# Kernel tuning notes

Measured on AMD Instinct MI355X. Metric: run time of the kernel, lower is better.

The kernel has to match this reference:

```python
import jax, jax.numpy as jnp
import numpy as np

B = 1024
D_FEAT = 64
WINDOW_SIZE = 8192
IR_SIZE = 1024
MAX_STEPS = 2799.0


def setup_inputs() -> dict:
    key = jax.random.key(0)
    ks = jax.random.split(key, 8)
    d_in = D_FEAT + 1  # vel_inputs concat K
    return {
        "vel_inputs": jax.random.normal(ks[0], (B, D_FEAT), dtype=jnp.float32),
        "K": jax.random.uniform(ks[1], (B, 1), dtype=jnp.float32) * MAX_STEPS,
        "eps": jax.random.normal(ks[2], (B, WINDOW_SIZE), dtype=jnp.float32),
        "W_coeff": jax.random.normal(ks[3], (d_in, WINDOW_SIZE), dtype=jnp.float32) * 0.02,
        "b_coeff": jnp.zeros((WINDOW_SIZE,), jnp.float32),
        "W_amps": jax.random.normal(ks[4], (d_in, 1), dtype=jnp.float32) * 0.02,
        "b_amps": jnp.zeros((1,), jnp.float32),
        "W_mean": jax.random.normal(ks[5], (d_in, 1), dtype=jnp.float32) * 0.02,
        "b_mean": jnp.zeros((1,), jnp.float32),
    }


def reference(vel_inputs, K, eps, W_coeff, b_coeff, W_amps, b_amps, W_mean, b_mean):
    # --- small MLP heads ---
    x = jnp.concatenate([vel_inputs, K / MAX_STEPS], axis=-1)  # [B, D+1]
    noise_bands = x @ W_coeff + b_coeff                        # [B, W] (magnitudes)
    amps = jax.nn.sigmoid(x @ W_amps + b_amps)                 # [B, 1]
    mean = jnp.tanh(x @ W_mean + b_mean)                       # [B, 1]

    # --- frequency_impulse_response: irfft + hann windowing (padding>0 branch) ---
    ir = jnp.fft.irfft(noise_bands, axis=-1)   # [B, 2*(W-1)] real
    ir = jnp.fft.fftshift(ir, axes=-1)
    ir_len = 2 * (WINDOW_SIZE - 1)             # 16382
    half = (IR_SIZE + 1) // 2                  # 512
    pad = ir_len - IR_SIZE                     # > 0 path
    n = jnp.arange(IR_SIZE, dtype=jnp.float32)
    hann = 0.5 - 0.5 * jnp.cos(2.0 * jnp.pi * n / IR_SIZE)  # tf periodic hann
    window = jnp.concatenate([hann[half:], jnp.zeros((pad,), jnp.float32), hann[:half]])
    ir = window * ir
    fhs = ir_len - (half - 1) + 1              # first_half_start
    she = half + 1                             # second_half_end
    impulse = jnp.concatenate([ir[:, fhs:], ir[:, :she]], axis=-1)  # [B, IR_SIZE-1]
    ir_final = impulse.shape[-1]               # 1023

    # --- noise generation (eps ~ N(0,1) injected for determinism) ---
    noise = mean + eps                         # [B, W]
    noise = noise / jnp.max(noise)             # global max, as in tf code

    # --- fft_convolve: original broadcasts to [B,B,...] then takes [0];
    # equivalent: noise row 0 convolved with every batch's impulse. ---
    conv_len = ir_final + WINDOW_SIZE - 1
    fft_size = int(2 ** np.ceil(np.log2(conv_len)))  # 16384
    a_fft = jnp.fft.rfft(noise[0], n=fft_size)          # [F]
    ir_fft = jnp.fft.rfft(impulse, n=fft_size, axis=-1)  # [B, F]
    conv = jnp.fft.irfft(a_fft[None, :] * ir_fft, axis=-1)  # [B, fft_size]

    # crop_and_compensate_delay ('same')
    start = (ir_final - 1) // 2 - 1            # 510
    cropped = conv[:, start:start + WINDOW_SIZE]  # [B, W]

    # overlap_and_add over a single frame with step W//2 is the identity
    out_noise = amps * cropped                 # [B, W]
    return out_noise, mean
```

## Files before the change

### kernel.cpp

```cpp
#include <hip/hip_runtime.h>
#include <math.h>

#define NB 1024
#define DF 64
#define WIN 8192
#define LIR 16382
#define TBASE 7681
#define NJ 1024
#define INV_MAXSTEPS (1.0f/2799.0f)
#define TWO_PI 6.28318530717958647692f

#define REVLEN 9248
#define SREV 8212

#define BW_ELEMS 1160
#define BW_CHUNKS 145

using short8 = __attribute__((ext_vector_type(8))) short;
using f32x4  = __attribute__((ext_vector_type(4))) float;

static __device__ __forceinline__ short f2bf(float x) {
    unsigned u = __float_as_uint(x);
    unsigned r = (u + 0x7fffu + ((u >> 16) & 1u)) >> 16;
    return (short)r;
}

#define PREP_CT_BLK 4096
#define PREP_W_BLK  320
#define PREP_H_BLK  4
__global__ __launch_bounds__(256) void k_prep(const float* __restrict__ Wc,
                                              const float* __restrict__ bc,
                                              const float* __restrict__ vel,
                                              const float* __restrict__ Kv,
                                              const float* __restrict__ Wa,
                                              const float* __restrict__ ba,
                                              const float* __restrict__ Wm,
                                              const float* __restrict__ bm,
                                              short* __restrict__ Ct,
                                              short* __restrict__ Waug,
                                              float* __restrict__ amps,
                                              float* __restrict__ mean,
                                              float* __restrict__ out_mean,
                                              unsigned* __restrict__ gmb) {
    int bx = blockIdx.x, tid = threadIdx.x;
    if (bx < PREP_CT_BLK) {
        int flat = bx * 2048 + tid * 8;
        int j = flat >> 13, k0 = flat & 8191;
        int t = TBASE + j;
        int p = (k0 * t) % LIR;
        float hw = 0.5f - 0.5f * __builtin_amdgcn_cosf((float)(j + 2) * (1.0f / 1024.0f));
        if (j == NJ - 1) hw = 0.0f;
        short8 v;
        #pragma unroll
        for (int e = 0; e < 8; ++e) {
            int k = k0 + e;
            float w = (k == 0 || k == LIR / 2) ? (1.0f / (float)LIR) : (2.0f / (float)LIR);
            float c = __builtin_amdgcn_cosf((float)p * (1.0f / (float)LIR)) * w * hw;
            v[e] = f2bf(c);
            p += t; if (p >= LIR) p -= LIR;
        }
        *(short8*)(Ct + flat) = v;
    } else if (bx < PREP_CT_BLK + PREP_W_BLK) {
        int flat = (bx - PREP_CT_BLK) * 2048 + tid * 8;
        int d = flat >> 13, k0 = flat & 8191;
        short8 v;
        #pragma unroll
        for (int e = 0; e < 8; ++e) {
            float x = 0.0f;
            if (d < 65)       x = Wc[(size_t)d * WIN + k0 + e];
            else if (d == 65) x = bc[k0 + e];
            v[e] = f2bf(x);
        }
        *(short8*)(Waug + flat) = v;
    } else if (bx < PREP_CT_BLK + PREP_W_BLK + PREP_H_BLK) {
        int b = (bx - PREP_CT_BLK - PREP_W_BLK) * 256 + tid;
        float sa = ba[0], sm = bm[0];
        #pragma unroll 8
        for (int d = 0; d < DF; ++d) {
            float v = vel[b * DF + d];
            sa = fmaf(v, Wa[d], sa);
            sm = fmaf(v, Wm[d], sm);
        }
        float xk = Kv[b] * INV_MAXSTEPS;
        sa = fmaf(xk, Wa[DF], sa);
        sm = fmaf(xk, Wm[DF], sm);
        amps[b] = 1.0f / (1.0f + expf(-sa));
        float m = tanhf(sm);
        mean[b] = m;
        out_mean[b] = m;
    } else {
        if (tid == 0) gmb[0] = 0u;
    }
}

__global__ void k_maxpart(const float* __restrict__ eps, const float* __restrict__ mean,
                          unsigned* __restrict__ gmb) {
    __shared__ float red[256];
    int tid = threadIdx.x;
    float m = -INFINITY;
    const int total4 = NB * WIN / 4;
    const int stride = 1024 * 256;
    const float4* e4 = (const float4*)eps;
    for (int idx = blockIdx.x * 256 + tid; idx < total4; idx += stride) {
        int b = idx >> 11;
        float4 v = e4[idx];
        float mm = fmaxf(fmaxf(v.x, v.y), fmaxf(v.z, v.w));
        m = fmaxf(m, mean[b] + mm);
    }
    red[tid] = m;
    __syncthreads();
    for (int s = 128; s > 0; s >>= 1) {
        if (tid < s) red[tid] = fmaxf(red[tid], red[tid + s]);
        __syncthreads();
    }
    if (tid == 0) {
        unsigned u = __float_as_uint(red[0]);
        unsigned key = (u & 0x80000000u) ? ~u : (u | 0x80000000u);
        atomicMax(gmb, key);
    }
}

__global__ void k_nrevm(const unsigned* __restrict__ gmb, const float* __restrict__ mean,
                        const float* __restrict__ eps, short* __restrict__ revc) {
    int c = blockIdx.y;
    int x = blockIdx.x * 256 + threadIdx.x;
    if (x >= REVLEN) return;
    unsigned key = gmb[0];
    unsigned u = (key & 0x80000000u) ? (key & 0x7FFFFFFFu) : ~key;
    float inv = 1.0f / __uint_as_float(u);
    float m0 = mean[0];
    int q = 9239 - x - c;
    int mm = q - 517;
    float v = ((unsigned)mm < (unsigned)WIN) ? (m0 + eps[mm]) * inv : 0.0f;
    revc[c * REVLEN + x] = f2bf(v);
}

__global__ __launch_bounds__(256) void k_gemmA(const short* __restrict__ Ct,
                                               const short* __restrict__ Waug,
                                               float* __restrict__ Apart) {
    __shared__ short sA[128 * 128];
    __shared__ short sB[80 * 128];
    int tid = threadIdx.x;
    int j0 = blockIdx.x * 128;
    int ky = blockIdx.y;
    int k0 = ky * 128;

    #pragma unroll
    for (int it = 0; it < 8; ++it) {
        int q = it * 256 + tid;
        int row = q >> 4, co = q & 15;
        float4 v = *(const float4*)(Ct + (size_t)(j0 + row) * WIN + k0 + co * 8);
        int db = row * 256 + ((co * 16) ^ ((row & 7) << 4));
        *(float4*)((char*)sA + db) = v;
    }
    #pragma unroll
    for (int it = 0; it < 5; ++it) {
        int q = it * 256 + tid;
        int row = q >> 4, co = q & 15;
        float4 v = *(const float4*)(Waug + (size_t)row * WIN + k0 + co * 8);
        int db = row * 256 + ((co * 16) ^ ((row & 7) << 4));
        *(float4*)((char*)sB + db) = v;
    }
    __syncthreads();

    int l = tid & 63, w = tid >> 6;
    int lm = l & 15, lg = l >> 4;

    f32x4 acc[2][5];
    #pragma unroll
    for (int mf = 0; mf < 2; ++mf)
        #pragma unroll
        for (int nf = 0; nf < 5; ++nf)
            #pragma unroll
            for (int r = 0; r < 4; ++r) acc[mf][nf][r] = 0.0f;

    #pragma unroll
    for (int kk = 0; kk < 4; ++kk) {
        int kb = kk * 64 + 16 * lg;
        short8 a[2], b[5];
        #pragma unroll
        for (int mf = 0; mf < 2; ++mf) {
            int row = w * 32 + mf * 16 + lm;
            a[mf] = *(const short8*)((char*)sA + row * 256 + (kb ^ ((row & 7) << 4)));
        }
        #pragma unroll
        for (int nf = 0; nf < 5; ++nf) {
            int d = nf * 16 + lm;
            b[nf] = *(const short8*)((char*)sB + d * 256 + (kb ^ ((d & 7) << 4)));
        }
        #pragma unroll
        for (int nf = 0; nf < 5; ++nf) {
            acc[0][nf] = __builtin_amdgcn_mfma_f32_16x16x32_bf16(a[0], b[nf], acc[0][nf], 0, 0, 0);
            acc[1][nf] = __builtin_amdgcn_mfma_f32_16x16x32_bf16(a[1], b[nf], acc[1][nf], 0, 0, 0);
        }
    }
    float* base = Apart + (size_t)ky * (NJ * 80);
    #pragma unroll
    for (int mf = 0; mf < 2; ++mf)
        #pragma unroll
        for (int r = 0; r < 4; ++r) {
            int j = j0 + w * 32 + mf * 16 + 4 * lg + r;
            #pragma unroll
            for (int nf = 0; nf < 5; ++nf)
                base[(size_t)j * 80 + nf * 16 + lm] = acc[mf][nf][r];
        }
}

__global__ __launch_bounds__(256) void k_red(const float* __restrict__ Apart,
                                             float* __restrict__ Aimp) {
    int flat = blockIdx.x * 256 + threadIdx.x;
    float s = 0.0f;
    #pragma unroll 8
    for (int ky = 0; ky < 64; ++ky)
        s += Apart[(size_t)ky * (NJ * 80) + flat];
    int j = flat / 80, d = flat - j * 80;
    Aimp[d * NJ + j] = s;
}

__global__ void k_imp(const float* __restrict__ Aimp, const float* __restrict__ vel,
                      const float* __restrict__ Kv, short* __restrict__ imp_bf) {
    int tid = threadIdx.x;
    int b0 = blockIdx.x * 4;
    float acc[4][4];
    #pragma unroll
    for (int bb = 0; bb < 4; ++bb)
        #pragma unroll
        for (int q = 0; q < 4; ++q) acc[bb][q] = 0.0f;
    for (int d = 0; d < 65; ++d) {
        float xv[4];
        #pragma unroll
        for (int bb = 0; bb < 4; ++bb)
            xv[bb] = (d < DF) ? vel[(b0 + bb) * DF + d] : Kv[b0 + bb] * INV_MAXSTEPS;
        #pragma unroll
        for (int q = 0; q < 4; ++q) {
            float av = Aimp[d * NJ + q * 256 + tid];
            #pragma unroll
            for (int bb = 0; bb < 4; ++bb)
                acc[bb][q] = fmaf(xv[bb], av, acc[bb][q]);
        }
    }
    #pragma unroll
    for (int q = 0; q < 4; ++q) {
        float av = Aimp[65 * NJ + q * 256 + tid];
        #pragma unroll
        for (int bb = 0; bb < 4; ++bb)
            imp_bf[(size_t)(b0 + bb) * NJ + q * 256 + tid] = f2bf(acc[bb][q] + av);
    }
}

__global__ __launch_bounds__(256) void k_gemm(const short* __restrict__ imp_bf,
                                              const short* __restrict__ revc,
                                              const float* __restrict__ amps,
                                              float* __restrict__ out) {
    __shared__ short sA[2][128 * 64];
    __shared__ short sB[8 * BW_ELEMS];
    int tid = threadIdx.x;
    int bid = blockIdx.x;
    int m_idx = bid & 7;
    int n_idx = bid >> 3;
    int brow0 = m_idx * 128;
    int icol0 = n_idx * 128;
    int wbase = 8080 - icol0;

    for (int q = tid; q < 8 * BW_CHUNKS; q += 256) {
        int c = q / BW_CHUNKS;
        int u8 = (q - c * BW_CHUNKS) * 8;
        *(float4*)(sB + q * 8) = *(const float4*)(revc + c * REVLEN + wbase + u8);
    }

    float4 st[4];
    #pragma unroll
    for (int it = 0; it < 4; ++it) {
        int q = it * 256 + tid;
        int row = q >> 3, c16 = q & 7;
        st[it] = *(const float4*)(imp_bf + (size_t)(brow0 + row) * NJ + c16 * 8);
    }
    #pragma unroll
    for (int it = 0; it < 4; ++it) {
        int q = it * 256 + tid;
        int row = q >> 3, c16 = q & 7;
        int db = row * 128 + ((c16 * 16) ^ ((row & 7) << 4));
        *(float4*)((char*)sA[0] + db) = st[it];
    }

    int l = tid & 63, w = tid >> 6;
    int wm = w >> 1, wn = w & 1;
    int lm = l & 15, lg = l >> 4;

    int aoff[4][2];
    #pragma unroll
    for (int mf = 0; mf < 4; ++mf)
        #pragma unroll
        for (int kki = 0; kki < 2; ++kki) {
            int row = wm * 64 + mf * 16 + lm;
            int kb = (kki * 32 + 8 * lg) * 2;
            aoff[mf][kki] = row * 64 + ((kb ^ ((row & 7) << 4)) >> 1);
        }
    int boff[4];
    #pragma unroll
    for (int nf = 0; nf < 4; ++nf) {
        int i = icol0 + wn * 64 + nf * 16 + lm;
        int snf = SREV - i;
        int c = snf & 7;
        boff[nf] = c * BW_ELEMS + (snf - c - wbase) + 8 * lg;
    }

    f32x4 acc[4][4];
    #pragma unroll
    for (int mf = 0; mf < 4; ++mf)
        #pragma unroll
        for (int nf = 0; nf < 4; ++nf)
            #pragma unroll
            for (int r = 0; r < 4; ++r) acc[mf][nf][r] = 0.0f;

    int p = 0;
    for (int ch = 0; ch < 16; ++ch) {
        __syncthreads();
        if (ch < 15) {
            int k0n = (ch + 1) * 64;
            #pragma unroll
            for (int it = 0; it < 4; ++it) {
                int q = it * 256 + tid;
                int row = q >> 3, c16 = q & 7;
                st[it] = *(const float4*)(imp_bf + (size_t)(brow0 + row) * NJ + k0n + c16 * 8);
            }
        }
        int k0 = ch * 64;
        #pragma unroll
        for (int kki = 0; kki < 2; ++kki) {
            short8 af[4], bfr[4];
            #pragma unroll
            for (int mf = 0; mf < 4; ++mf)
                af[mf] = *(const short8*)(sA[p] + aoff[mf][kki]);
            #pragma unroll
            for (int nf = 0; nf < 4; ++nf)
                bfr[nf] = *(const short8*)(sB + boff[nf] + k0 + kki * 32);
            #pragma unroll
            for (int mf = 0; mf < 4; ++mf)
                #pragma unroll
                for (int nf = 0; nf < 4; ++nf)
                    acc[mf][nf] = __builtin_amdgcn_mfma_f32_16x16x32_bf16(
                        af[mf], bfr[nf], acc[mf][nf], 0, 0, 0);
        }
        if (ch < 15) {
            #pragma unroll
            for (int it = 0; it < 4; ++it) {
                int q = it * 256 + tid;
                int row = q >> 3, c16 = q & 7;
                int db = row * 128 + ((c16 * 16) ^ ((row & 7) << 4));
                *(float4*)((char*)sA[p ^ 1] + db) = st[it];
            }
        }
        p ^= 1;
    }

    #pragma unroll
    for (int mf = 0; mf < 4; ++mf) {
        #pragma unroll
        for (int r = 0; r < 4; ++r) {
            int row = brow0 + wm * 64 + mf * 16 + 4 * lg + r;
            float a = amps[row];
            #pragma unroll
            for (int nf = 0; nf < 4; ++nf)
                out[(size_t)row * WIN + icol0 + wn * 64 + nf * 16 + lm] = a * acc[mf][nf][r];
        }
    }
}

extern "C" void kernel_launch(void* const* d_in, const int* in_sizes, int n_in,
                              void* d_out, int out_size, void* d_ws, size_t ws_size,
                              hipStream_t stream) {
    const float* vel = (const float*)d_in[0];
    const float* Kv  = (const float*)d_in[1];
    const float* eps = (const float*)d_in[2];
    const float* Wc  = (const float*)d_in[3];
    const float* bc  = (const float*)d_in[4];
    const float* Wa  = (const float*)d_in[5];
    const float* ba  = (const float*)d_in[6];
    const float* Wm  = (const float*)d_in[7];
    const float* bm  = (const float*)d_in[8];
    float* out = (float*)d_out;

    char* ws = (char*)d_ws;
    float*    amps   = (float*)(ws + 0);
    float*    mean   = (float*)(ws + 4096);
    unsigned* gmb    = (unsigned*)(ws + 8192);
    float*    Aimp   = (float*)(ws + 16384);
    short*    imp_bf = (short*)(ws + 344064);
    short*    Waug   = (short*)(ws + 2441216);
    short*    revc   = (short*)(ws + 3751936);
    short*    Ct     = (short*)(ws + 4194304);
    float*    Apart  = (float*)(ws + 20971520);

    k_prep   <<<dim3(PREP_CT_BLK + PREP_W_BLK + PREP_H_BLK + 1), dim3(256), 0, stream>>>(
                 Wc, bc, vel, Kv, Wa, ba, Wm, bm, Ct, Waug,
                 amps, mean, out + (size_t)NB * WIN, gmb);
    k_maxpart<<<dim3(1024),   dim3(256), 0, stream>>>(eps, mean, gmb);
    k_nrevm  <<<dim3(37, 8),  dim3(256), 0, stream>>>(gmb, mean, eps, revc);
    k_gemmA  <<<dim3(8, 64),  dim3(256), 0, stream>>>(Ct, Waug, Apart);
    k_red    <<<dim3(320),    dim3(256), 0, stream>>>(Apart, Aimp);
    k_imp    <<<dim3(256),    dim3(256), 0, stream>>>(Aimp, vel, Kv, imp_bf);
    k_gemm   <<<dim3(512),    dim3(256), 0, stream>>>(imp_bf, revc, amps, out);
}
```

Before: 166.8 us.

## Generate cosine basis on the fly inside GEMM, fuse reduction with noise prep

```diff
diff --git a/kernel.cpp b/kernel.cpp
--- a/kernel.cpp
+++ b/kernel.cpp
@@ -8,13 +8,14 @@
 #define TBASE 7681
 #define NJ 1024
 #define INV_MAXSTEPS (1.0f/2799.0f)
-#define TWO_PI 6.28318530717958647692f
 
 #define REVLEN 9248
 #define SREV 8212
 
 #define BW_ELEMS 1160
 #define BW_CHUNKS 145
+
+#define KY 32
 
 using short8 = __attribute__((ext_vector_type(8))) short;
 using f32x4  = __attribute__((ext_vector_type(4))) float;
@@ -25,72 +26,139 @@
     return (short)r;
 }
 
-#define PREP_CT_BLK 4096
-#define PREP_W_BLK  320
-#define PREP_H_BLK  4
-__global__ __launch_bounds__(256) void k_prep(const float* __restrict__ Wc,
-                                              const float* __restrict__ bc,
-                                              const float* __restrict__ vel,
-                                              const float* __restrict__ Kv,
-                                              const float* __restrict__ Wa,
-                                              const float* __restrict__ ba,
-                                              const float* __restrict__ Wm,
-                                              const float* __restrict__ bm,
-                                              short* __restrict__ Ct,
-                                              short* __restrict__ Waug,
-                                              float* __restrict__ amps,
-                                              float* __restrict__ mean,
-                                              float* __restrict__ out_mean,
-                                              unsigned* __restrict__ gmb) {
+__global__ __launch_bounds__(256) void k_A(const float* __restrict__ Wc,
+                                           const float* __restrict__ bc,
+                                           const float* __restrict__ vel,
+                                           const float* __restrict__ Kv,
+                                           const float* __restrict__ Wa,
+                                           const float* __restrict__ ba,
+                                           const float* __restrict__ Wm,
+                                           const float* __restrict__ bm,
+                                           float* __restrict__ Apart,
+                                           float* __restrict__ amps,
+                                           float* __restrict__ mean,
+                                           float* __restrict__ out_mean,
+                                           unsigned* __restrict__ gmb) {
+    __shared__ short sA[128 * 128];
+    __shared__ short sB[80 * 128];
     int bx = blockIdx.x, tid = threadIdx.x;
-    if (bx < PREP_CT_BLK) {
-        int flat = bx * 2048 + tid * 8;
-        int j = flat >> 13, k0 = flat & 8191;
-        int t = TBASE + j;
-        int p = (k0 * t) % LIR;
-        float hw = 0.5f - 0.5f * __builtin_amdgcn_cosf((float)(j + 2) * (1.0f / 1024.0f));
-        if (j == NJ - 1) hw = 0.0f;
-        short8 v;
-        #pragma unroll
-        for (int e = 0; e < 8; ++e) {
-            int k = k0 + e;
-            float w = (k == 0 || k == LIR / 2) ? (1.0f / (float)LIR) : (2.0f / (float)LIR);
-            float c = __builtin_amdgcn_cosf((float)p * (1.0f / (float)LIR)) * w * hw;
-            v[e] = f2bf(c);
-            p += t; if (p >= LIR) p -= LIR;
-        }
-        *(short8*)(Ct + flat) = v;
-    } else if (bx < PREP_CT_BLK + PREP_W_BLK) {
-        int flat = (bx - PREP_CT_BLK) * 2048 + tid * 8;
-        int d = flat >> 13, k0 = flat & 8191;
-        short8 v;
-        #pragma unroll
-        for (int e = 0; e < 8; ++e) {
-            float x = 0.0f;
-            if (d < 65)       x = Wc[(size_t)d * WIN + k0 + e];
-            else if (d == 65) x = bc[k0 + e];
-            v[e] = f2bf(x);
-        }
-        *(short8*)(Waug + flat) = v;
-    } else if (bx < PREP_CT_BLK + PREP_W_BLK + PREP_H_BLK) {
-        int b = (bx - PREP_CT_BLK - PREP_W_BLK) * 256 + tid;
-        float sa = ba[0], sm = bm[0];
-        #pragma unroll 8
-        for (int d = 0; d < DF; ++d) {
-            float v = vel[b * DF + d];
-            sa = fmaf(v, Wa[d], sa);
-            sm = fmaf(v, Wm[d], sm);
-        }
-        float xk = Kv[b] * INV_MAXSTEPS;
-        sa = fmaf(xk, Wa[DF], sa);
-        sm = fmaf(xk, Wm[DF], sm);
-        amps[b] = 1.0f / (1.0f + expf(-sa));
-        float m = tanhf(sm);
-        mean[b] = m;
-        out_mean[b] = m;
-    } else {
-        if (tid == 0) gmb[0] = 0u;
-    }
+
+    if (bx >= 256) {
+        if (bx < 260) {
+            int b = (bx - 256) * 256 + tid;
+            float sa = ba[0], sm = bm[0];
+            #pragma unroll 8
+            for (int d = 0; d < DF; ++d) {
+                float v = vel[b * DF + d];
+                sa = fmaf(v, Wa[d], sa);
+                sm = fmaf(v, Wm[d], sm);
+            }
+            float xk = Kv[b] * INV_MAXSTEPS;
+            sa = fmaf(xk, Wa[DF], sa);
+            sm = fmaf(xk, Wm[DF], sm);
+            amps[b] = 1.0f / (1.0f + expf(-sa));
+            float m = tanhf(sm);
+            mean[b] = m;
+            out_mean[b] = m;
+        } else if (tid == 0) {
+            gmb[0] = 0u;
+        }
+        return;
+    }
+
+    int m_idx = bx & 7, kyb = bx >> 3;
+    int j0 = m_idx * 128;
+    int l = tid & 63, w = tid >> 6;
+    int lm = l & 15, lg = l >> 4;
+
+    f32x4 acc[2][5];
+    #pragma unroll
+    for (int mf = 0; mf < 2; ++mf)
+        #pragma unroll
+        for (int nf = 0; nf < 5; ++nf)
+            #pragma unroll
+            for (int r = 0; r < 4; ++r) acc[mf][nf][r] = 0.0f;
+
+    for (int half = 0; half < 2; ++half) {
+        int k0 = (kyb * 2 + half) * 128;
+        __syncthreads();
+
+        #pragma unroll
+        for (int it = 0; it < 8; ++it) {
+            int q = it * 256 + tid;
+            int row = q >> 4, co = q & 15;
+            int j = j0 + row;
+            int t = TBASE + j;
+            int k = k0 + co * 8;
+            int p = (k * t) % LIR;
+            float hw = 0.5f - 0.5f * __builtin_amdgcn_cosf((float)(j + 2) * (1.0f / 1024.0f));
+            if (j == NJ - 1) hw = 0.0f;
+            short8 v;
+            #pragma unroll
+            for (int e = 0; e < 8; ++e) {
+                int kk = k + e;
+                float wk = (kk == 0 || kk == LIR / 2) ? (1.0f / (float)LIR) : (2.0f / (float)LIR);
+                float c = __builtin_amdgcn_cosf((float)p * (1.0f / (float)LIR)) * wk * hw;
+                v[e] = f2bf(c);
+                p += t; if (p >= LIR) p -= LIR;
+            }
+            int db = row * 256 + ((co * 16) ^ ((row & 7) << 4));
+            *(short8*)((char*)sA + db) = v;
+        }
+        #pragma unroll
+        for (int it = 0; it < 5; ++it) {
+            int q = it * 256 + tid;
+            int row = q >> 4, co = q & 15;
+            short8 v;
+            if (row < 65) {
+                const float* src = Wc + (size_t)row * WIN + k0 + co * 8;
+                #pragma unroll
+                for (int e = 0; e < 8; ++e) v[e] = f2bf(src[e]);
+            } else if (row == 65) {
+                const float* src = bc + k0 + co * 8;
+                #pragma unroll
+                for (int e = 0; e < 8; ++e) v[e] = f2bf(src[e]);
+            } else {
+                #pragma unroll
+                for (int e = 0; e < 8; ++e) v[e] = 0;
+            }
+            int db = row * 256 + ((co * 16) ^ ((row & 7) << 4));
+            *(short8*)((char*)sB + db) = v;
+        }
+        __syncthreads();
+
+        #pragma unroll
+        for (int kk = 0; kk < 4; ++kk) {
+            int kb = kk * 64 + 16 * lg;
+            short8 a[2], b[5];
+            #pragma unroll
+            for (int mf = 0; mf < 2; ++mf) {
+                int row = w * 32 + mf * 16 + lm;
+                a[mf] = *(const short8*)((char*)sA + row * 256 + (kb ^ ((row & 7) << 4)));
+            }
+            #pragma unroll
+            for (int nf = 0; nf < 5; ++nf) {
+                int d = nf * 16 + lm;
+                b[nf] = *(const short8*)((char*)sB + d * 256 + (kb ^ ((d & 7) << 4)));
+            }
+            #pragma unroll
+            for (int nf = 0; nf < 5; ++nf) {
+                acc[0][nf] = __builtin_amdgcn_mfma_f32_16x16x32_bf16(a[0], b[nf], acc[0][nf], 0, 0, 0);
+                acc[1][nf] = __builtin_amdgcn_mfma_f32_16x16x32_bf16(a[1], b[nf], acc[1][nf], 0, 0, 0);
+            }
+        }
+    }
+
+    float* base = Apart + (size_t)kyb * (NJ * 80);
+    #pragma unroll
+    for (int mf = 0; mf < 2; ++mf)
+        #pragma unroll
+        for (int r = 0; r < 4; ++r) {
+            int j = j0 + w * 32 + mf * 16 + 4 * lg + r;
+            #pragma unroll
+            for (int nf = 0; nf < 5; ++nf)
+                base[(size_t)j * 80 + nf * 16 + lm] = acc[mf][nf][r];
+        }
 }
 
 __global__ void k_maxpart(const float* __restrict__ eps, const float* __restrict__ mean,
@@ -120,101 +188,35 @@
     }
 }
 
-__global__ void k_nrevm(const unsigned* __restrict__ gmb, const float* __restrict__ mean,
-                        const float* __restrict__ eps, short* __restrict__ revc) {
-    int c = blockIdx.y;
-    int x = blockIdx.x * 256 + threadIdx.x;
-    if (x >= REVLEN) return;
-    unsigned key = gmb[0];
-    unsigned u = (key & 0x80000000u) ? (key & 0x7FFFFFFFu) : ~key;
-    float inv = 1.0f / __uint_as_float(u);
-    float m0 = mean[0];
-    int q = 9239 - x - c;
-    int mm = q - 517;
-    float v = ((unsigned)mm < (unsigned)WIN) ? (m0 + eps[mm]) * inv : 0.0f;
-    revc[c * REVLEN + x] = f2bf(v);
-}
-
-__global__ __launch_bounds__(256) void k_gemmA(const short* __restrict__ Ct,
-                                               const short* __restrict__ Waug,
-                                               float* __restrict__ Apart) {
-    __shared__ short sA[128 * 128];
-    __shared__ short sB[80 * 128];
-    int tid = threadIdx.x;
-    int j0 = blockIdx.x * 128;
-    int ky = blockIdx.y;
-    int k0 = ky * 128;
-
-    #pragma unroll
-    for (int it = 0; it < 8; ++it) {
-        int q = it * 256 + tid;
-        int row = q >> 4, co = q & 15;
-        float4 v = *(const float4*)(Ct + (size_t)(j0 + row) * WIN + k0 + co * 8);
-        int db = row * 256 + ((co * 16) ^ ((row & 7) << 4));
-        *(float4*)((char*)sA + db) = v;
-    }
-    #pragma unroll
-    for (int it = 0; it < 5; ++it) {
-        int q = it * 256 + tid;
-        int row = q >> 4, co = q & 15;
-        float4 v = *(const float4*)(Waug + (size_t)row * WIN + k0 + co * 8);
-        int db = row * 256 + ((co * 16) ^ ((row & 7) << 4));
-        *(float4*)((char*)sB + db) = v;
-    }
-    __syncthreads();
-
-    int l = tid & 63, w = tid >> 6;
-    int lm = l & 15, lg = l >> 4;
-
-    f32x4 acc[2][5];
-    #pragma unroll
-    for (int mf = 0; mf < 2; ++mf)
-        #pragma unroll
-        for (int nf = 0; nf < 5; ++nf)
-            #pragma unroll
-            for (int r = 0; r < 4; ++r) acc[mf][nf][r] = 0.0f;
-
-    #pragma unroll
-    for (int kk = 0; kk < 4; ++kk) {
-        int kb = kk * 64 + 16 * lg;
-        short8 a[2], b[5];
-        #pragma unroll
-        for (int mf = 0; mf < 2; ++mf) {
-            int row = w * 32 + mf * 16 + lm;
-            a[mf] = *(const short8*)((char*)sA + row * 256 + (kb ^ ((row & 7) << 4)));
-        }
-        #pragma unroll
-        for (int nf = 0; nf < 5; ++nf) {
-            int d = nf * 16 + lm;
-            b[nf] = *(const short8*)((char*)sB + d * 256 + (kb ^ ((d & 7) << 4)));
-        }
-        #pragma unroll
-        for (int nf = 0; nf < 5; ++nf) {
-            acc[0][nf] = __builtin_amdgcn_mfma_f32_16x16x32_bf16(a[0], b[nf], acc[0][nf], 0, 0, 0);
-            acc[1][nf] = __builtin_amdgcn_mfma_f32_16x16x32_bf16(a[1], b[nf], acc[1][nf], 0, 0, 0);
-        }
-    }
-    float* base = Apart + (size_t)ky * (NJ * 80);
-    #pragma unroll
-    for (int mf = 0; mf < 2; ++mf)
-        #pragma unroll
-        for (int r = 0; r < 4; ++r) {
-            int j = j0 + w * 32 + mf * 16 + 4 * lg + r;
-            #pragma unroll
-            for (int nf = 0; nf < 5; ++nf)
-                base[(size_t)j * 80 + nf * 16 + lm] = acc[mf][nf][r];
-        }
-}
-
-__global__ __launch_bounds__(256) void k_red(const float* __restrict__ Apart,
-                                             float* __restrict__ Aimp) {
-    int flat = blockIdx.x * 256 + threadIdx.x;
-    float s = 0.0f;
-    #pragma unroll 8
-    for (int ky = 0; ky < 64; ++ky)
-        s += Apart[(size_t)ky * (NJ * 80) + flat];
-    int j = flat / 80, d = flat - j * 80;
-    Aimp[d * NJ + j] = s;
+__global__ __launch_bounds__(256) void k_rednrev(const float* __restrict__ Apart,
+                                                 float* __restrict__ Aimp,
+                                                 const unsigned* __restrict__ gmb,
+                                                 const float* __restrict__ mean,
+                                                 const float* __restrict__ eps,
+                                                 short* __restrict__ revc) {
+    int bx = blockIdx.x, tid = threadIdx.x;
+    if (bx < 320) {
+        int flat = bx * 256 + tid;
+        float s = 0.0f;
+        #pragma unroll 8
+        for (int ky = 0; ky < KY; ++ky)
+            s += Apart[(size_t)ky * (NJ * 80) + flat];
+        int j = flat / 80, d = flat - j * 80;
+        Aimp[d * NJ + j] = s;
+    } else {
+        int r = bx - 320;
+        int c = r / 37, xb = r - c * 37;
+        int x = xb * 256 + tid;
+        if (x >= REVLEN) return;
+        unsigned key = gmb[0];
+        unsigned u = (key & 0x80000000u) ? (key & 0x7FFFFFFFu) : ~key;
+        float inv = 1.0f / __uint_as_float(u);
+        float m0 = mean[0];
+        int q = 9239 - x - c;
+        int mm = q - 517;
+        float v = ((unsigned)mm < (unsigned)WIN) ? (m0 + eps[mm]) * inv : 0.0f;
+        revc[c * REVLEN + x] = f2bf(v);
+    }
 }
 
 __global__ void k_imp(const float* __restrict__ Aimp, const float* __restrict__ vel,
@@ -387,18 +389,14 @@
     unsigned* gmb    = (unsigned*)(ws + 8192);
     float*    Aimp   = (float*)(ws + 16384);
     short*    imp_bf = (short*)(ws + 344064);
-    short*    Waug   = (short*)(ws + 2441216);
-    short*    revc   = (short*)(ws + 3751936);
-    short*    Ct     = (short*)(ws + 4194304);
-    float*    Apart  = (float*)(ws + 20971520);
-
-    k_prep   <<<dim3(PREP_CT_BLK + PREP_W_BLK + PREP_H_BLK + 1), dim3(256), 0, stream>>>(
-                 Wc, bc, vel, Kv, Wa, ba, Wm, bm, Ct, Waug,
-                 amps, mean, out + (size_t)NB * WIN, gmb);
-    k_maxpart<<<dim3(1024),   dim3(256), 0, stream>>>(eps, mean, gmb);
-    k_nrevm  <<<dim3(37, 8),  dim3(256), 0, stream>>>(gmb, mean, eps, revc);
-    k_gemmA  <<<dim3(8, 64),  dim3(256), 0, stream>>>(Ct, Waug, Apart);
-    k_red    <<<dim3(320),    dim3(256), 0, stream>>>(Apart, Aimp);
-    k_imp    <<<dim3(256),    dim3(256), 0, stream>>>(Aimp, vel, Kv, imp_bf);
-    k_gemm   <<<dim3(512),    dim3(256), 0, stream>>>(imp_bf, revc, amps, out);
-}
+    short*    revc   = (short*)(ws + 2441216);
+    float*    Apart  = (float*)(ws + 2592768);
+
+    k_A      <<<dim3(261),  dim3(256), 0, stream>>>(Wc, bc, vel, Kv, Wa, ba, Wm, bm,
+                                                    Apart, amps, mean,
+                                                    out + (size_t)NB * WIN, gmb);
+    k_maxpart<<<dim3(1024), dim3(256), 0, stream>>>(eps, mean, gmb);
+    k_rednrev<<<dim3(616),  dim3(256), 0, stream>>>(Apart, Aimp, gmb, mean, eps, revc);
+    k_imp    <<<dim3(256),  dim3(256), 0, stream>>>(Aimp, vel, Kv, imp_bf);
+    k_gemm   <<<dim3(512),  dim3(256), 0, stream>>>(imp_bf, revc, amps, out);
+}
```

Result: faster. 154.4 us (-7.4%).
